# Optimization experiments

Hardware: AMD Instinct MI355X
Metric: run time of the kernel (lower is better)

Reference implementation:

```python
import jax, jax.numpy as jnp
import numpy as np

NEG_SLOPE = 0.01  # torch LeakyReLU default

def leaky_relu(x):
    return jnp.where(x >= 0, x, NEG_SLOPE * x)

def gcn_conv(h, W, b, src, dst, n):
    # PyG GCNConv: linear (no bias), add self-loops, symmetric norm, scatter-add, + bias
    h = h @ W  # [N, F]
    loop = jnp.arange(n, dtype=src.dtype)
    s = jnp.concatenate([src, loop])
    d = jnp.concatenate([dst, loop])
    deg = jax.ops.segment_sum(jnp.ones_like(d, dtype=h.dtype), d, num_segments=n)
    dinv = jnp.where(deg > 0, deg ** -0.5, 0.0)
    norm = dinv[s] * dinv[d]  # [E+N]
    msg = h[s] * norm[:, None]
    out = jax.ops.segment_sum(msg, d, num_segments=n)
    return out + b

def setup_inputs() -> dict:
    key = jax.random.key(0)
    ks = jax.random.split(key, 12)
    N, E, D_IN, D_H, D_OUT, C = 100000, 3200000, 512, 128, 64, 2
    def lin(k, fi, fo):
        bound = 1.0 / np.sqrt(fi)
        k1, k2 = jax.random.split(k)
        W = jax.random.uniform(k1, (fi, fo), jnp.float32, -bound, bound)
        b = jax.random.uniform(k2, (fo,), jnp.float32, -bound, bound)
        return W, b
    W1, b1 = lin(ks[0], D_IN, D_H)
    W2, b2 = lin(ks[1], D_H, D_OUT)
    Wg1, bg1 = lin(ks[2], D_OUT, D_OUT)
    Wg2, bg2 = lin(ks[3], D_OUT, D_OUT)
    Wc, bc = lin(ks[4], D_OUT, C)
    x = jax.random.normal(ks[5], (N, D_IN), jnp.float32)
    edge_index = jax.random.randint(ks[6], (2, E), 0, N, jnp.int32)
    return {"x": x, "edge_index": edge_index, "W1": W1, "b1": b1, "W2": W2, "b2": b2,
            "Wg1": Wg1, "bg1": bg1, "Wg2": Wg2, "bg2": bg2, "Wc": Wc, "bc": bc}

def reference(x, edge_index, W1, b1, W2, b2, Wg1, bg1, Wg2, bg2, Wc, bc):
    n = x.shape[0]
    src, dst = edge_index[0], edge_index[1]
    # encoder (dropout = identity in eval)
    h = leaky_relu(x @ W1 + b1)
    h = leaky_relu(h @ W2 + b2)
    # two GCN layers
    h = leaky_relu(gcn_conv(h, Wg1, bg1, src, dst, n))
    h = leaky_relu(gcn_conv(h, Wg2, bg2, src, dst, n))
    logits = h @ Wc + bc
    return logits, h
```

## Files before the change

### kernel.cpp

```cpp
#include <hip/hip_runtime.h>
#include <hip/hip_bf16.h>

typedef __bf16 v8bf16 __attribute__((ext_vector_type(8)));
typedef float  v4f32  __attribute__((ext_vector_type(4)));
typedef unsigned short ushort8v __attribute__((ext_vector_type(8)));

static __device__ __forceinline__ float leaky(float v) { return v >= 0.0f ? v : 0.01f * v; }
static __device__ __forceinline__ float bfbits2f(unsigned short b) {
    union { unsigned u; float f; } c; c.u = ((unsigned)b) << 16; return c.f;
}
static __device__ __forceinline__ unsigned short f2bfbits(float f) {
    __hip_bfloat16 h = __float2bfloat16(f);
    unsigned short s; __builtin_memcpy(&s, &h, 2); return s;
}

constexpr int EPB  = 6400;
constexpr int BCAP = 16384;

__global__ __launch_bounds__(256) void prep_all(
    const float* __restrict__ W1, const float* __restrict__ W2,
    const float* __restrict__ Wg1, const float* __restrict__ Wg2,
    __hip_bfloat16* __restrict__ W1f, __hip_bfloat16* __restrict__ W2t,
    __hip_bfloat16* __restrict__ Wg1t, __hip_bfloat16* __restrict__ Wg2t,
    unsigned* __restrict__ bcur, int DIN, int DH, int DO, int NB) {
    const int fragTotal  = DIN * DH;
    const int fragBlocks = (fragTotal + 255) / 256;
    const int n2 = DH * DO, ng = DO * DO;
    const int smallTotal  = n2 + 2 * ng;
    const int smallBlocks = (smallTotal + 255) / 256;
    const int bid = blockIdx.x;
    if (bid < fragBlocks) {
        int tid = bid * 256 + threadIdx.x;
        if (tid >= fragTotal) return;
        int j = tid & 7, l = (tid >> 3) & 63, G = tid >> 9;
        int m = l & 15, q = l >> 4;
        int t = G & 7, kk = G >> 3;
        int n = t * 16 + m;
        int k = kk * 32 + q * 8 + j;
        W1f[tid] = __float2bfloat16(W1[k * DH + n]);
    } else if (bid < fragBlocks + smallBlocks) {
        int i = (bid - fragBlocks) * 256 + threadIdx.x;
        if (i < n2) {
            int r = i / DO, c = i % DO;
            W2t[c * DH + r] = __float2bfloat16(W2[i]);
        } else if (i < n2 + ng) {
            int j = i - n2; int r = j / DO, c = j % DO;
            Wg1t[c * DO + r] = __float2bfloat16(Wg1[j]);
        } else if (i < smallTotal) {
            int j = i - n2 - ng; int r = j / DO, c = j % DO;
            Wg2t[c * DO + r] = __float2bfloat16(Wg2[j]);
        }
    } else {
        int i = (bid - fragBlocks - smallBlocks) * 256 + threadIdx.x;
        if (i < NB) bcur[i] = 0u;
    }
}

struct ScatterSmem {
    unsigned stg[EPB];
    unsigned hist[512], inc[512], cur[512], start[512];
};

static __device__ __forceinline__ void scatter_body(
    int bid, ScatterSmem& sm, const int* __restrict__ src, const int* __restrict__ dst,
    unsigned* __restrict__ bcur, unsigned* __restrict__ ebuck, int E, int NB) {
    const int tid = threadIdx.x;
    sm.hist[tid] = 0u;
    __syncthreads();
    const int beg = bid * EPB;
    const int end = min(beg + EPB, E);
    for (int e = beg + tid; e < end; e += 512)
        atomicAdd(&sm.hist[((unsigned)dst[e]) >> 8], 1u);
    __syncthreads();
    const unsigned h = sm.hist[tid];
    sm.inc[tid] = h;
    __syncthreads();
    for (int off = 1; off < 512; off <<= 1) {
        unsigned t = (tid >= off) ? sm.inc[tid - off] : 0u;
        __syncthreads();
        sm.inc[tid] += t;
        __syncthreads();
    }
    sm.cur[tid] = sm.inc[tid] - h;
    if (tid < NB && h > 0u)
        sm.start[tid] = (unsigned)tid * BCAP + atomicAdd(&bcur[tid], h);
    __syncthreads();
    for (int e = beg + tid; e < end; e += 512) {
        unsigned b = ((unsigned)dst[e]) >> 8;
        unsigned r = atomicAdd(&sm.cur[b], 1u);
        sm.stg[r] = (unsigned)e;
    }
    __syncthreads();
    const int cnt = end - beg;
    for (int s = tid; s < cnt; s += 512) {
        const unsigned e = sm.stg[s];
        const unsigned d = (unsigned)dst[e];
        const unsigned b = d >> 8;
        const unsigned excl = sm.inc[b] - sm.hist[b];
        const unsigned pos = sm.start[b] + ((unsigned)s - excl);
        ebuck[pos] = (unsigned)src[e] | ((d & 255u) << 20);
    }
}

static __device__ __forceinline__ void enc1_body(
    int bid, uint4 (*lds)[1024], const float* __restrict__ A, const uint4* __restrict__ Bp,
    const float* __restrict__ bias, __hip_bfloat16* __restrict__ C, int M) {
    constexpr int K = 512;
    const int tid = threadIdx.x;
    const int wid = tid >> 6, lane = tid & 63;
    const int m = lane & 15, q = lane >> 4;
    const int row0 = bid * 128 + wid * 16;
    const int rowA = row0 + m;
    const int rowAc = rowA < M ? rowA : M - 1;
    const float* Ap = A + (size_t)rowAc * K + q * 8;

    v4f32 acc[8];
#pragma unroll
    for (int t = 0; t < 8; t++) acc[t] = (v4f32){0.f, 0.f, 0.f, 0.f};

    float4 ab[2][4];

    auto loadA = [&](int c, int par) {
#pragma unroll
        for (int j = 0; j < 4; j++)
            ab[par][j] = *reinterpret_cast<const float4*>(Ap + c * 64 + (j >> 1) * 32 + (j & 1) * 4);
    };
    auto stage = [&](int c, int par) {
        lds[par][tid]       = Bp[c * 1024 + tid];
        lds[par][512 + tid] = Bp[c * 1024 + 512 + tid];
    };

    stage(0, 0);
    loadA(0, 0);
    for (int c = 0; c < 8; c++) {
        __syncthreads();
        if (c < 7) { stage(c + 1, (c + 1) & 1); loadA(c + 1, (c + 1) & 1); }
        const int par = c & 1;
#pragma unroll
        for (int kk2 = 0; kk2 < 2; kk2++) {
            float4 f0 = ab[par][kk2 * 2], f1 = ab[par][kk2 * 2 + 1];
            v8bf16 a = {(__bf16)f0.x, (__bf16)f0.y, (__bf16)f0.z, (__bf16)f0.w,
                        (__bf16)f1.x, (__bf16)f1.y, (__bf16)f1.z, (__bf16)f1.w};
#pragma unroll
            for (int t = 0; t < 8; t++) {
                v8bf16 b = reinterpret_cast<const v8bf16*>(lds[par])[(kk2 * 8 + t) * 64 + lane];
                acc[t] = __builtin_amdgcn_mfma_f32_16x16x32_bf16(a, b, acc[t], 0, 0, 0);
            }
        }
    }

#pragma unroll
    for (int r = 0; r < 4; r++) {
        const int row = row0 + q * 4 + r;
        if (row >= M) continue;
#pragma unroll
        for (int t = 0; t < 8; t++) {
            const int col = t * 16 + m;
            C[(size_t)row * 128 + col] = __float2bfloat16(leaky(acc[t][r] + bias[col]));
        }
    }
}

__global__ __launch_bounds__(512, 4) void mega_scatter_enc1(
    const int* __restrict__ src, const int* __restrict__ dst,
    unsigned* __restrict__ bcur, unsigned* __restrict__ ebuck, int E, int NB, int nScatter,
    const float* __restrict__ A, const uint4* __restrict__ Bp,
    const float* __restrict__ bias, __hip_bfloat16* __restrict__ C, int M) {
    union Smem {
        ScatterSmem sc;
        uint4 g[2][1024];
    };
    __shared__ Smem sm;
    const int bid = blockIdx.x;
    if (bid < nScatter) scatter_body(bid, sm.sc, src, dst, bcur, ebuck, E, NB);
    else                enc1_body(bid - nScatter, sm.g, A, Bp, bias, C, M);
}

template <int NT, int MODE>
static __device__ __forceinline__ void gemm_body(
    int bid, const __hip_bfloat16* __restrict__ A, const __hip_bfloat16* __restrict__ Bt,
    const float* __restrict__ bias, const float* __restrict__ dinv,
    __hip_bfloat16* __restrict__ Cbf, int M, int K) {
    const int wid  = threadIdx.x >> 6;
    const int lane = threadIdx.x & 63;
    const int row0 = (bid * 4 + wid) << 4;
    if (row0 >= M) return;
    const int m = lane & 15, q = lane >> 4;

    const __hip_bfloat16* Ab = A + (size_t)(row0 + m) * K + q * 8;

    v4f32 acc[NT];
#pragma unroll
    for (int t = 0; t < NT; t++) acc[t] = (v4f32){0.f, 0.f, 0.f, 0.f};

    for (int k0 = 0; k0 < K; k0 += 32) {
        v8bf16 a = *reinterpret_cast<const v8bf16*>(Ab + k0);
#pragma unroll
        for (int t = 0; t < NT; t++) {
            v8bf16 b = *reinterpret_cast<const v8bf16*>(Bt + (size_t)(t * 16 + m) * K + k0 + q * 8);
            acc[t] = __builtin_amdgcn_mfma_f32_16x16x32_bf16(a, b, acc[t], 0, 0, 0);
        }
    }

    const int N = NT * 16;
#pragma unroll
    for (int r = 0; r < 4; r++) {
        const int row = row0 + q * 4 + r;
        float di = (MODE == 1) ? dinv[row] : 1.0f;
#pragma unroll
        for (int t = 0; t < NT; t++) {
            const int col = t * 16 + m;
            float v = acc[t][r];
            if (MODE == 0) v = leaky(v + bias[col]);
            else           v *= di;
            Cbf[(size_t)row * N + col] = __float2bfloat16(v);
        }
    }
}

template <int NT, int MODE>
__global__ __launch_bounds__(256) void gemm_kernel(
    const __hip_bfloat16* __restrict__ A, const __hip_bfloat16* __restrict__ Bt,
    const float* __restrict__ bias, const float* __restrict__ dinv,
    __hip_bfloat16* __restrict__ Cbf, int M, int K) {
    gemm_body<NT, MODE>(blockIdx.x, A, Bt, bias, dinv, Cbf, M, K);
}

static __device__ __forceinline__ void csr_body(
    int k, unsigned* hist, unsigned* cur, const unsigned* __restrict__ bcur,
    const unsigned* __restrict__ ebuck, uint2* __restrict__ rp2,
    float* __restrict__ dinv, int* __restrict__ csr, int NN) {
    const int tid = threadIdx.x;
    const unsigned cntb = bcur[k];
    const unsigned base = (unsigned)k * BCAP;
    const unsigned* eb = ebuck + base;
    hist[tid] = 0u;
    __syncthreads();
    for (unsigned e = tid; e < cntb; e += 256)
        atomicAdd(&hist[eb[e] >> 20], 1u);
    __syncthreads();
    const unsigned h = hist[tid];
    cur[tid] = h;
    __syncthreads();
    for (int off = 1; off < 256; off <<= 1) {
        unsigned t = (tid >= off) ? cur[tid - off] : 0u;
        __syncthreads();
        cur[tid] += t;
        __syncthreads();
    }
    const unsigned excl = cur[tid] - h;
    const int node = k * 256 + tid;
    if (node < NN) {
        rp2[node] = make_uint2(base + excl, base + excl + h);
        dinv[node] = rsqrtf((float)(h + 1u));
    }
    __syncthreads();
    cur[tid] = excl;
    __syncthreads();
    for (unsigned e = tid; e < cntb; e += 256) {
        const unsigned pk = eb[e];
        const unsigned pos = base + atomicAdd(&cur[pk >> 20], 1u);
        csr[pos] = (int)(pk & 0xFFFFFu);
    }
}

__global__ __launch_bounds__(256) void mega_csr_enc2(
    const unsigned* __restrict__ bcur, const unsigned* __restrict__ ebuck,
    uint2* __restrict__ rp2, float* __restrict__ dinv, int* __restrict__ csr,
    int NN, int nCsr,
    const __hip_bfloat16* __restrict__ A, const __hip_bfloat16* __restrict__ Bt,
    const float* __restrict__ bias, __hip_bfloat16* __restrict__ Cb, int M, int K) {
    __shared__ unsigned hist[256], cur[256];
    const int bid = blockIdx.x;
    if (bid < nCsr) csr_body(bid, hist, cur, bcur, ebuck, rp2, dinv, csr, NN);
    else            gemm_body<4, 0>(bid - nCsr, A, Bt, bias, nullptr, Cb, M, K);
}

template <int HEAD>
__global__ __launch_bounds__(256) void gather_kernel(
    const uint2* __restrict__ rp2, const int* __restrict__ csr_src,
    const __hip_bfloat16* __restrict__ u, const float* __restrict__ dinv,
    const float* __restrict__ bias, __hip_bfloat16* __restrict__ out_bf,
    float* __restrict__ out_h, const float* __restrict__ Wc,
    const float* __restrict__ bc, float* __restrict__ out_logits, int n) {
    const int node = blockIdx.x * 4 + (threadIdx.x >> 6);
    if (node >= n) return;
    const int lane = threadIdx.x & 63;
    const int g = lane >> 3, t = lane & 7;
    const uint2 rp = rp2[node];
    const unsigned beg = rp.x, end = rp.y;

    float s[8];
#pragma unroll
    for (int j = 0; j < 8; j++) s[j] = 0.f;

    unsigned e = beg + g;
    bool hA = e < end, hB = e + 8 < end;
    int sA = hA ? csr_src[e] : 0;
    int sB = hB ? csr_src[e + 8] : 0;
    while (hA) {
        const unsigned en = e + 16;
        const bool hA2 = en < end, hB2 = en + 8 < end;
        const int sA2 = hA2 ? csr_src[en] : 0;
        const int sB2 = hB2 ? csr_src[en + 8] : 0;
        ushort8v wA = *reinterpret_cast<const ushort8v*>(u + (size_t)sA * 64 + t * 8);
        if (hB) {
            ushort8v wB = *reinterpret_cast<const ushort8v*>(u + (size_t)sB * 64 + t * 8);
#pragma unroll
            for (int j = 0; j < 8; j++) s[j] += bfbits2f(wA[j]) + bfbits2f(wB[j]);
        } else {
#pragma unroll
            for (int j = 0; j < 8; j++) s[j] += bfbits2f(wA[j]);
        }
        e = en; hA = hA2; hB = hB2; sA = sA2; sB = sB2;
    }
#pragma unroll
    for (int j = 0; j < 8; j++) {
        s[j] += __shfl_xor(s[j], 8, 64);
        s[j] += __shfl_xor(s[j], 16, 64);
        s[j] += __shfl_xor(s[j], 32, 64);
    }

    ushort8v wsr = *reinterpret_cast<const ushort8v*>(u + (size_t)node * 64 + t * 8);
#pragma unroll
    for (int j = 0; j < 8; j++) s[j] += bfbits2f(wsr[j]);

    const float di = dinv[node];
    const float4 b0 = *reinterpret_cast<const float4*>(bias + t * 8);
    const float4 b1 = *reinterpret_cast<const float4*>(bias + t * 8 + 4);
    float f[8];
    f[0] = leaky(s[0] * di + b0.x); f[1] = leaky(s[1] * di + b0.y);
    f[2] = leaky(s[2] * di + b0.z); f[3] = leaky(s[3] * di + b0.w);
    f[4] = leaky(s[4] * di + b1.x); f[5] = leaky(s[5] * di + b1.y);
    f[6] = leaky(s[6] * di + b1.z); f[7] = leaky(s[7] * di + b1.w);

    if (HEAD == 0) {
        if (g == 0) {
            ushort8v o;
#pragma unroll
            for (int j = 0; j < 8; j++) o[j] = f2bfbits(f[j]);
            *reinterpret_cast<ushort8v*>(out_bf + (size_t)node * 64 + t * 8) = o;
        }
    } else {
        if (g == 0) {
            float4 o0 = {f[0], f[1], f[2], f[3]};
            float4 o1 = {f[4], f[5], f[6], f[7]};
            *reinterpret_cast<float4*>(out_h + (size_t)node * 64 + t * 8) = o0;
            *reinterpret_cast<float4*>(out_h + (size_t)node * 64 + t * 8 + 4) = o1;
        }
        float p0 = 0.f, p1 = 0.f;
#pragma unroll
        for (int j = 0; j < 8; j++) {
            p0 += f[j] * Wc[(t * 8 + j) * 2];
            p1 += f[j] * Wc[(t * 8 + j) * 2 + 1];
        }
#pragma unroll
        for (int o = 4; o; o >>= 1) {
            p0 += __shfl_xor(p0, o, 64);
            p1 += __shfl_xor(p1, o, 64);
        }
        if (lane == 0) {
            out_logits[(size_t)node * 2 + 0] = p0 + bc[0];
            out_logits[(size_t)node * 2 + 1] = p1 + bc[1];
        }
    }
}

extern "C" void kernel_launch(void* const* d_in, const int* in_sizes, int n_in,
                              void* d_out, int out_size, void* d_ws, size_t ws_size,
                              hipStream_t stream) {
    const float* x   = (const float*)d_in[0];
    const int*   ei  = (const int*)d_in[1];
    const float* W1  = (const float*)d_in[2];
    const float* b1  = (const float*)d_in[3];
    const float* W2  = (const float*)d_in[4];
    const float* b2  = (const float*)d_in[5];
    const float* Wg1 = (const float*)d_in[6];
    const float* bg1 = (const float*)d_in[7];
    const float* Wg2 = (const float*)d_in[8];
    const float* bg2 = (const float*)d_in[9];
    const float* Wc  = (const float*)d_in[10];
    const float* bc  = (const float*)d_in[11];

    const int DH  = in_sizes[3];
    const int DIN = in_sizes[2] / DH;
    const int NN  = in_sizes[0] / DIN;
    const int E   = in_sizes[1] / 2;
    const int DO  = in_sizes[5];
    const int* src = ei;
    const int* dst = ei + E;

    char*  ws  = (char*)d_ws;
    size_t off = 0;
    auto alloc = [&](size_t bytes) {
        void* p = ws + off;
        off += (bytes + 255) & ~(size_t)255;
        return p;
    };
    const int NB = (NN + 255) >> 8;
    __hip_bfloat16* h1    = (__hip_bfloat16*)alloc((size_t)NN * DH * 2);
    __hip_bfloat16* h2    = (__hip_bfloat16*)alloc((size_t)NN * DO * 2);
    __hip_bfloat16* h3    = (__hip_bfloat16*)alloc((size_t)NN * DO * 2);
    __hip_bfloat16* ub    = (__hip_bfloat16*)alloc((size_t)NN * DO * 2);
    float*          dinv  = (float*)alloc((size_t)NN * 4);
    uint2*          rp2   = (uint2*)alloc((size_t)NN * 8);
    int*            csr   = (int*)alloc((size_t)NB * BCAP * 4);
    unsigned*       ebuck = (unsigned*)alloc((size_t)NB * BCAP * 4);
    unsigned*       bcur  = (unsigned*)alloc(512 * 4);
    __hip_bfloat16* W1f   = (__hip_bfloat16*)alloc((size_t)DIN * DH * 2);
    __hip_bfloat16* W2t   = (__hip_bfloat16*)alloc((size_t)DH * DO * 2);
    __hip_bfloat16* Wg1t  = (__hip_bfloat16*)alloc((size_t)DO * DO * 2);
    __hip_bfloat16* Wg2t  = (__hip_bfloat16*)alloc((size_t)DO * DO * 2);

    float* out_logits = (float*)d_out;
    float* out_h      = (float*)d_out + (size_t)NN * 2;

    const int fragBlocks  = (DIN * DH + 255) / 256;
    const int smallBlocks = (DH * DO + 2 * DO * DO + 255) / 256;
    const int zeroBlocks  = (NB + 255) / 256;
    prep_all<<<fragBlocks + smallBlocks + zeroBlocks, 256, 0, stream>>>(
        W1, W2, Wg1, Wg2, W1f, W2t, Wg1t, Wg2t, bcur, DIN, DH, DO, NB);

    const int nblkP = (E + EPB - 1) / EPB;
    const int enc1B = (NN + 127) / 128;
    mega_scatter_enc1<<<nblkP + enc1B, 512, 0, stream>>>(
        src, dst, bcur, ebuck, E, NB, nblkP,
        x, (const uint4*)W1f, b1, h1, NN);

    const int gemm_blocks = (NN / 16 + 3) / 4;
    mega_csr_enc2<<<NB + gemm_blocks, 256, 0, stream>>>(
        bcur, ebuck, rp2, dinv, csr, NN, NB,
        h1, W2t, b2, h2, NN, DH);

    gemm_kernel<4, 1><<<gemm_blocks, 256, 0, stream>>>(h2, Wg1t, nullptr, dinv, ub, NN, DO);
    gather_kernel<0><<<(NN + 3) / 4, 256, 0, stream>>>(rp2, csr, ub, dinv, bg1, h3,
                                                       nullptr, nullptr, nullptr, nullptr, NN);

    gemm_kernel<4, 1><<<gemm_blocks, 256, 0, stream>>>(h3, Wg2t, nullptr, dinv, ub, NN, DO);
    gather_kernel<1><<<(NN + 3) / 4, 256, 0, stream>>>(rp2, csr, ub, dinv, bg2, nullptr,
                                                       out_h, Wc, bc, out_logits, NN);
}
```

Baseline: 557.1 us.

## Fuse second GCN linear into first gather, interleave block roles, cache dst in registers

The first gather kernel now applies the Wg2 matmul per node in fp32 through lane shuffles and scales the result by dinv, writing the pre-normalised features straight to a buffer. This removes the second GEMM launch, the h3 intermediate round trip and the Wg2 transpose prep. Both mega-kernels also spread their two block roles evenly across the grid instead of placing one role first, aiming for better overlap. The scatter pass keeps its 13 dst values per thread in registers so dst is not read from global memory a second time. The risks are an extra 64-term FMA loop with shuffles in every gather wavefront and more register pressure in the scatter body.

```diff
diff --git a/kernel.cpp b/kernel.cpp
--- a/kernel.cpp
+++ b/kernel.cpp
@@ -17,16 +17,24 @@
 constexpr int EPB  = 6400;
 constexpr int BCAP = 16384;
 
+static __device__ __forceinline__ bool role_split(int bid, int nA, int tot,
+                                                  int& idxA, int& idxB) {
+    const long long s0 = (long long)bid * nA / tot;
+    const long long s1 = (long long)(bid + 1) * nA / tot;
+    if (s1 > s0) { idxA = (int)s0; idxB = 0; return true; }
+    idxA = 0; idxB = bid - (int)s0; return false;
+}
+
 __global__ __launch_bounds__(256) void prep_all(
     const float* __restrict__ W1, const float* __restrict__ W2,
-    const float* __restrict__ Wg1, const float* __restrict__ Wg2,
+    const float* __restrict__ Wg1,
     __hip_bfloat16* __restrict__ W1f, __hip_bfloat16* __restrict__ W2t,
-    __hip_bfloat16* __restrict__ Wg1t, __hip_bfloat16* __restrict__ Wg2t,
+    __hip_bfloat16* __restrict__ Wg1t,
     unsigned* __restrict__ bcur, int DIN, int DH, int DO, int NB) {
     const int fragTotal  = DIN * DH;
     const int fragBlocks = (fragTotal + 255) / 256;
     const int n2 = DH * DO, ng = DO * DO;
-    const int smallTotal  = n2 + 2 * ng;
+    const int smallTotal  = n2 + ng;
     const int smallBlocks = (smallTotal + 255) / 256;
     const int bid = blockIdx.x;
     if (bid < fragBlocks) {
@@ -43,12 +51,9 @@
         if (i < n2) {
             int r = i / DO, c = i % DO;
             W2t[c * DH + r] = __float2bfloat16(W2[i]);
-        } else if (i < n2 + ng) {
+        } else if (i < smallTotal) {
             int j = i - n2; int r = j / DO, c = j % DO;
             Wg1t[c * DO + r] = __float2bfloat16(Wg1[j]);
-        } else if (i < smallTotal) {
-            int j = i - n2 - ng; int r = j / DO, c = j % DO;
-            Wg2t[c * DO + r] = __float2bfloat16(Wg2[j]);
         }
     } else {
         int i = (bid - fragBlocks - smallBlocks) * 256 + threadIdx.x;
@@ -69,8 +74,16 @@
     __syncthreads();
     const int beg = bid * EPB;
     const int end = min(beg + EPB, E);
-    for (int e = beg + tid; e < end; e += 512)
-        atomicAdd(&sm.hist[((unsigned)dst[e]) >> 8], 1u);
+    unsigned myd[13];
+#pragma unroll
+    for (int i = 0; i < 13; i++) {
+        const int e = beg + tid + i * 512;
+        if (e < end) {
+            const unsigned d = (unsigned)dst[e];
+            myd[i] = d;
+            atomicAdd(&sm.hist[d >> 8], 1u);
+        }
+    }
     __syncthreads();
     const unsigned h = sm.hist[tid];
     sm.inc[tid] = h;
@@ -85,10 +98,14 @@
     if (tid < NB && h > 0u)
         sm.start[tid] = (unsigned)tid * BCAP + atomicAdd(&bcur[tid], h);
     __syncthreads();
-    for (int e = beg + tid; e < end; e += 512) {
-        unsigned b = ((unsigned)dst[e]) >> 8;
-        unsigned r = atomicAdd(&sm.cur[b], 1u);
-        sm.stg[r] = (unsigned)e;
+#pragma unroll
+    for (int i = 0; i < 13; i++) {
+        const int e = beg + tid + i * 512;
+        if (e < end) {
+            const unsigned b = myd[i] >> 8;
+            const unsigned r = atomicAdd(&sm.cur[b], 1u);
+            sm.stg[r] = (unsigned)e;
+        }
     }
     __syncthreads();
     const int cnt = end - beg;
@@ -171,9 +188,11 @@
         uint4 g[2][1024];
     };
     __shared__ Smem sm;
-    const int bid = blockIdx.x;
-    if (bid < nScatter) scatter_body(bid, sm.sc, src, dst, bcur, ebuck, E, NB);
-    else                enc1_body(bid - nScatter, sm.g, A, Bp, bias, C, M);
+    int ia, ib;
+    if (role_split(blockIdx.x, nScatter, gridDim.x, ia, ib))
+        scatter_body(ia, sm.sc, src, dst, bcur, ebuck, E, NB);
+    else
+        enc1_body(ib, sm.g, A, Bp, bias, C, M);
 }
 
 template <int NT, int MODE>
@@ -271,9 +290,11 @@
     const __hip_bfloat16* __restrict__ A, const __hip_bfloat16* __restrict__ Bt,
     const float* __restrict__ bias, __hip_bfloat16* __restrict__ Cb, int M, int K) {
     __shared__ unsigned hist[256], cur[256];
-    const int bid = blockIdx.x;
-    if (bid < nCsr) csr_body(bid, hist, cur, bcur, ebuck, rp2, dinv, csr, NN);
-    else            gemm_body<4, 0>(bid - nCsr, A, Bt, bias, nullptr, Cb, M, K);
+    int ia, ib;
+    if (role_split(blockIdx.x, nCsr, gridDim.x, ia, ib))
+        csr_body(ia, hist, cur, bcur, ebuck, rp2, dinv, csr, NN);
+    else
+        gemm_body<4, 0>(ib, A, Bt, bias, nullptr, Cb, M, K);
 }
 
 template <int HEAD>
@@ -281,7 +302,7 @@
     const uint2* __restrict__ rp2, const int* __restrict__ csr_src,
     const __hip_bfloat16* __restrict__ u, const float* __restrict__ dinv,
     const float* __restrict__ bias, __hip_bfloat16* __restrict__ out_bf,
-    float* __restrict__ out_h, const float* __restrict__ Wc,
+    float* __restrict__ out_h, const float* __restrict__ Wmid,
     const float* __restrict__ bc, float* __restrict__ out_logits, int n) {
     const int node = blockIdx.x * 4 + (threadIdx.x >> 6);
     if (node >= n) return;
@@ -335,12 +356,15 @@
     f[6] = leaky(s[6] * di + b1.z); f[7] = leaky(s[7] * di + b1.w);
 
     if (HEAD == 0) {
-        if (g == 0) {
-            ushort8v o;
-#pragma unroll
-            for (int j = 0; j < 8; j++) o[j] = f2bfbits(f[j]);
-            *reinterpret_cast<ushort8v*>(out_bf + (size_t)node * 64 + t * 8) = o;
-        }
+        float a0 = 0.f, a1 = 0.f;
+#pragma unroll
+        for (int j = 0; j < 64; j += 2) {
+            const float r0 = __shfl(f[j & 7], j >> 3, 64);
+            const float r1 = __shfl(f[(j + 1) & 7], (j + 1) >> 3, 64);
+            a0 += r0 * Wmid[j * 64 + lane];
+            a1 += r1 * Wmid[(j + 1) * 64 + lane];
+        }
+        out_bf[(size_t)node * 64 + lane] = __float2bfloat16((a0 + a1) * di);
     } else {
         if (g == 0) {
             float4 o0 = {f[0], f[1], f[2], f[3]};
@@ -351,8 +375,8 @@
         float p0 = 0.f, p1 = 0.f;
 #pragma unroll
         for (int j = 0; j < 8; j++) {
-            p0 += f[j] * Wc[(t * 8 + j) * 2];
-            p1 += f[j] * Wc[(t * 8 + j) * 2 + 1];
+            p0 += f[j] * Wmid[(t * 8 + j) * 2];
+            p1 += f[j] * Wmid[(t * 8 + j) * 2 + 1];
         }
 #pragma unroll
         for (int o = 4; o; o >>= 1) {
@@ -400,8 +424,8 @@
     const int NB = (NN + 255) >> 8;
     __hip_bfloat16* h1    = (__hip_bfloat16*)alloc((size_t)NN * DH * 2);
     __hip_bfloat16* h2    = (__hip_bfloat16*)alloc((size_t)NN * DO * 2);
-    __hip_bfloat16* h3    = (__hip_bfloat16*)alloc((size_t)NN * DO * 2);
     __hip_bfloat16* ub    = (__hip_bfloat16*)alloc((size_t)NN * DO * 2);
+    __hip_bfloat16* ub2   = (__hip_bfloat16*)alloc((size_t)NN * DO * 2);
     float*          dinv  = (float*)alloc((size_t)NN * 4);
     uint2*          rp2   = (uint2*)alloc((size_t)NN * 8);
     int*            csr   = (int*)alloc((size_t)NB * BCAP * 4);
@@ -410,16 +434,15 @@
     __hip_bfloat16* W1f   = (__hip_bfloat16*)alloc((size_t)DIN * DH * 2);
     __hip_bfloat16* W2t   = (__hip_bfloat16*)alloc((size_t)DH * DO * 2);
     __hip_bfloat16* Wg1t  = (__hip_bfloat16*)alloc((size_t)DO * DO * 2);
-    __hip_bfloat16* Wg2t  = (__hip_bfloat16*)alloc((size_t)DO * DO * 2);
 
     float* out_logits = (float*)d_out;
     float* out_h      = (float*)d_out + (size_t)NN * 2;
 
     const int fragBlocks  = (DIN * DH + 255) / 256;
-    const int smallBlocks = (DH * DO + 2 * DO * DO + 255) / 256;
+    const int smallBlocks = (DH * DO + DO * DO + 255) / 256;
     const int zeroBlocks  = (NB + 255) / 256;
     prep_all<<<fragBlocks + smallBlocks + zeroBlocks, 256, 0, stream>>>(
-        W1, W2, Wg1, Wg2, W1f, W2t, Wg1t, Wg2t, bcur, DIN, DH, DO, NB);
+        W1, W2, Wg1, W1f, W2t, Wg1t, bcur, DIN, DH, DO, NB);
 
     const int nblkP = (E + EPB - 1) / EPB;
     const int enc1B = (NN + 127) / 128;
@@ -433,10 +456,8 @@
         h1, W2t, b2, h2, NN, DH);
 
     gemm_kernel<4, 1><<<gemm_blocks, 256, 0, stream>>>(h2, Wg1t, nullptr, dinv, ub, NN, DO);
-    gather_kernel<0><<<(NN + 3) / 4, 256, 0, stream>>>(rp2, csr, ub, dinv, bg1, h3,
-                                                       nullptr, nullptr, nullptr, nullptr, NN);
-
-    gemm_kernel<4, 1><<<gemm_blocks, 256, 0, stream>>>(h3, Wg2t, nullptr, dinv, ub, NN, DO);
-    gather_kernel<1><<<(NN + 3) / 4, 256, 0, stream>>>(rp2, csr, ub, dinv, bg2, nullptr,
+    gather_kernel<0><<<(NN + 3) / 4, 256, 0, stream>>>(rp2, csr, ub, dinv, bg1, ub2,
+                                                       nullptr, Wg2, nullptr, nullptr, NN);
+    gather_kernel<1><<<(NN + 3) / 4, 256, 0, stream>>>(rp2, csr, ub2, dinv, bg2, nullptr,
                                                        out_h, Wc, bc, out_logits, NN);
 }
```

After: 580.9 us. +4.3%, slower.
